# Optimization experiments

Measured on AMD Instinct MI355X. Metric: run time of the kernel, lower is better.

## Reference

```python
import jax, jax.numpy as jnp
import numpy as np

B, S, D, H = 64, 32, 1024, 1024


def setup_inputs() -> dict:
    key = jax.random.key(0)
    ks = jax.random.split(key, 12)
    sd = 1.0 / np.sqrt(D)
    sh = 1.0 / np.sqrt(H)
    return {
        "local_descs_t": jax.random.normal(ks[0], (B, S, D), jnp.float32),
        "local_descs_rot": jax.random.normal(ks[1], (B, S, D), jnp.float32),
        "scene_w": jax.random.normal(ks[2], (2 * D,), jnp.float32) * sd,
        "scene_b": jax.random.normal(ks[3], (1,), jnp.float32),
        "Wt1": jax.random.normal(ks[4], (S, D, H), jnp.float32) * sd,
        "bt1": jax.random.normal(ks[5], (S, H), jnp.float32) * 0.01,
        "Wt2": jax.random.normal(ks[6], (S, H, 3), jnp.float32) * sh,
        "bt2": jax.random.normal(ks[7], (S, 3), jnp.float32) * 0.01,
        "Wr1": jax.random.normal(ks[8], (S, D, H), jnp.float32) * sd,
        "br1": jax.random.normal(ks[9], (S, H), jnp.float32) * 0.01,
        "Wr2": jax.random.normal(ks[10], (S, H, 4), jnp.float32) * sh,
        "br2": jax.random.normal(ks[11], (S, 4), jnp.float32) * 0.01,
    }


def _pose_head(g, idx, W1, b1, W2, b2):
    # g: [B, D]; gather per-sample expert weights and run 2-layer MLP (GELU, exact erf as in F.gelu)
    h = jax.nn.gelu(jnp.einsum("bd,bdh->bh", g, W1[idx]) + b1[idx], approximate=False)
    return jnp.einsum("bh,bho->bo", h, W2[idx]) + b2[idx]


def reference(local_descs_t, local_descs_rot, scene_w, scene_b,
              Wt1, bt1, Wt2, bt2, Wr1, br1, Wr2, br2):
    # scene classification: Linear(2D -> 1) over concat descriptors, log-softmax over scenes
    logits = jnp.einsum("bsd,d->bs",
                        jnp.concatenate([local_descs_t, local_descs_rot], axis=2),
                        scene_w) + scene_b  # [B, S]
    scene_log_distr = jax.nn.log_softmax(logits, axis=1)
    idx = jnp.argmax(scene_log_distr, axis=1)  # top-1 scene per sample, [B]
    # select the chosen scene's descriptor (equivalent to one-hot mask * descs, summed over scenes)
    global_desc_t = jnp.take_along_axis(local_descs_t, idx[:, None, None], axis=1)[:, 0]    # [B, D]
    global_desc_rot = jnp.take_along_axis(local_descs_rot, idx[:, None, None], axis=1)[:, 0]
    # per-sample expert head dispatch (use_prior=False)
    x_t = _pose_head(global_desc_t, idx, Wt1, bt1, Wt2, bt2)      # [B, 3]
    x_rot = _pose_head(global_desc_rot, idx, Wr1, br1, Wr2, br2)  # [B, 4]
    expected_pose = jnp.concatenate([x_t, x_rot], axis=1)          # [B, 7]
    return expected_pose, scene_log_distr
```

## Files before the change

### kernel.cpp

```cpp
#include <hip/hip_runtime.h>
#include <math.h>

#define BB 64
#define SS 32
#define DD 1024
#define HH 1024
#define NG 40
#define GG 8

__device__ __forceinline__ float gelu_exact(float x) {
    return 0.5f * x * (1.0f + erff(x * 0.7071067811865476f));
}

#define WS_LOGITS 256
#define WS_GSCENE 8448
#define WS_GSAMP  8704
#define WS_PART   32768

__global__ __launch_bounds__(256) void logits_kernel(
    const float* __restrict__ descs_t, const float* __restrict__ descs_rot,
    const float* __restrict__ scene_w, float* __restrict__ logits)
{
    const int s = blockIdx.x, b = blockIdx.y;
    const int tid = threadIdx.x, lane = tid & 63, wave = tid >> 6;

    const float4* t4 = (const float4*)(descs_t  + ((size_t)b * SS + s) * DD);
    const float4* r4 = (const float4*)(descs_rot + ((size_t)b * SS + s) * DD);
    const float4* w4t = (const float4*)(scene_w);
    const float4* w4r = (const float4*)(scene_w + DD);

    float4 a = t4[tid], w = w4t[tid];
    float acc = a.x*w.x + a.y*w.y + a.z*w.z + a.w*w.w;
    float4 a2 = r4[tid], w2 = w4r[tid];
    acc += a2.x*w2.x + a2.y*w2.y + a2.z*w2.z + a2.w*w2.w;

    #pragma unroll
    for (int off = 32; off >= 1; off >>= 1) acc += __shfl_xor(acc, off, 64);

    __shared__ float red[4];
    if (lane == 0) red[wave] = acc;
    __syncthreads();
    if (tid == 0) logits[b * SS + s] = red[0] + red[1] + red[2] + red[3];
}

__global__ __launch_bounds__(64) void finalize_scene_kernel(
    const float* __restrict__ scene_b, float* __restrict__ logits,
    int* __restrict__ idx_ws, int* __restrict__ grp_scene, int* __restrict__ grp_samp,
    float* __restrict__ out)
{
    const int b = threadIdx.x;
    const float bias = scene_b[0];
    float lg[SS];
    float m = -1e30f; int am = 0;
    #pragma unroll
    for (int s = 0; s < SS; ++s) {
        lg[s] = logits[b * SS + s] + bias;
        if (lg[s] > m) { m = lg[s]; am = s; }
    }
    float sum = 0.f;
    #pragma unroll
    for (int s = 0; s < SS; ++s) sum += expf(lg[s] - m);
    const float lse = m + logf(sum);
    #pragma unroll
    for (int s = 0; s < SS; ++s) out[BB * 7 + b * SS + s] = lg[s] - lse;
    idx_ws[b] = am;

    __shared__ int sh_cnt[SS];
    __shared__ int sh_base[SS];
    __shared__ int sh_scene[NG];
    __shared__ int sh_samp[NG][GG];

    for (int i = b; i < NG; i += 64) sh_scene[i] = -1;
    for (int i = b; i < NG * GG; i += 64) ((int*)sh_samp)[i] = -1;

    int rank = 0;
    for (int s = 0; s < SS; ++s) {
        unsigned long long mk = __ballot(am == s);
        if (am == s) rank = __popcll(mk & ((1ull << b) - 1ull));
        if (b == s) sh_cnt[s] = (int)__popcll(mk);
    }
    __syncthreads();
    if (b == 0) {
        int acc = 0;
        for (int s = 0; s < SS; ++s) {
            sh_base[s] = acc;
            acc += (sh_cnt[s] + GG - 1) / GG;
        }
    }
    __syncthreads();
    {
        const int g = sh_base[am] + rank / GG;
        const int slot = rank % GG;
        sh_samp[g][slot] = b;
        if (slot == 0) sh_scene[g] = am;
    }
    __syncthreads();
    for (int i = b; i < NG; i += 64) grp_scene[i] = sh_scene[i];
    for (int i = b; i < NG * GG; i += 64) grp_samp[i] = ((int*)sh_samp)[i];
}

template<int DSPL>
__global__ __launch_bounds__(256) void layer1_kernel(
    const float* __restrict__ descs_t, const float* __restrict__ descs_rot,
    const float* __restrict__ Wt1, const float* __restrict__ Wr1,
    const int* __restrict__ grp_scene, const int* __restrict__ grp_samp,
    float* __restrict__ part)
{
    constexpr int DS = DD / DSPL;
    const int dsp  = blockIdx.x;
    const int g    = blockIdx.y;
    const int head = blockIdx.z;
    const int tid  = threadIdx.x;

    const int s = grp_scene[g];
    if (s < 0) return;

    __shared__ int   sh_b[GG];
    __shared__ float sh_g[DS][GG];
    if (tid < GG) sh_b[tid] = grp_samp[g * GG + tid];
    __syncthreads();

    const float* descs = head ? descs_rot : descs_t;
    for (int t = tid; t < GG * (DS / 4); t += 256) {
        const int p = t / (DS / 4);
        const int c = t % (DS / 4);
        const int b = sh_b[p];
        float4 v = make_float4(0.f, 0.f, 0.f, 0.f);
        if (b >= 0)
            v = ((const float4*)(descs + ((size_t)b * SS + s) * DD + dsp * DS))[c];
        sh_g[c * 4 + 0][p] = v.x;
        sh_g[c * 4 + 1][p] = v.y;
        sh_g[c * 4 + 2][p] = v.z;
        sh_g[c * 4 + 3][p] = v.w;
    }
    __syncthreads();

    const float* W = (head ? Wr1 : Wt1)
                   + (size_t)s * DD * HH + (size_t)dsp * DS * HH + tid * 4;

    float4 acc[GG];
    #pragma unroll
    for (int p = 0; p < GG; ++p) acc[p] = make_float4(0.f, 0.f, 0.f, 0.f);

    for (int d0 = 0; d0 < DS; d0 += 8) {
        float4 w[8];
        #pragma unroll
        for (int r = 0; r < 8; ++r)
            w[r] = *(const float4*)(W + (size_t)(d0 + r) * HH);
        #pragma unroll
        for (int r = 0; r < 8; ++r) {
            const float4 ga = *(const float4*)&sh_g[d0 + r][0];
            const float4 gb = *(const float4*)&sh_g[d0 + r][4];
            acc[0].x += ga.x*w[r].x; acc[0].y += ga.x*w[r].y; acc[0].z += ga.x*w[r].z; acc[0].w += ga.x*w[r].w;
            acc[1].x += ga.y*w[r].x; acc[1].y += ga.y*w[r].y; acc[1].z += ga.y*w[r].z; acc[1].w += ga.y*w[r].w;
            acc[2].x += ga.z*w[r].x; acc[2].y += ga.z*w[r].y; acc[2].z += ga.z*w[r].z; acc[2].w += ga.z*w[r].w;
            acc[3].x += ga.w*w[r].x; acc[3].y += ga.w*w[r].y; acc[3].z += ga.w*w[r].z; acc[3].w += ga.w*w[r].w;
            acc[4].x += gb.x*w[r].x; acc[4].y += gb.x*w[r].y; acc[4].z += gb.x*w[r].z; acc[4].w += gb.x*w[r].w;
            acc[5].x += gb.y*w[r].x; acc[5].y += gb.y*w[r].y; acc[5].z += gb.y*w[r].z; acc[5].w += gb.y*w[r].w;
            acc[6].x += gb.z*w[r].x; acc[6].y += gb.z*w[r].y; acc[6].z += gb.z*w[r].z; acc[6].w += gb.z*w[r].w;
            acc[7].x += gb.w*w[r].x; acc[7].y += gb.w*w[r].y; acc[7].z += gb.w*w[r].z; acc[7].w += gb.w*w[r].w;
        }
    }

    #pragma unroll
    for (int p = 0; p < GG; ++p) {
        const int b = sh_b[p];
        if (b >= 0) {
            float* dst = part + (((size_t)(head * BB + b) * DSPL + dsp) * HH) + tid * 4;
            *(float4*)dst = acc[p];
        }
    }
}

template<int DSPL>
__global__ __launch_bounds__(256) void head_out_kernel(
    const float* __restrict__ bt1, const float* __restrict__ Wt2, const float* __restrict__ bt2,
    const float* __restrict__ br1, const float* __restrict__ Wr2, const float* __restrict__ br2,
    const int* __restrict__ idx_ws, const float* __restrict__ part,
    float* __restrict__ out)
{
    const int b   = blockIdx.x;
    const int tid = threadIdx.x;
    const int s   = idx_ws[b];

    __shared__ float sh_h[2][HH];
    __shared__ float sh_red[7][4];

    #pragma unroll
    for (int head = 0; head < 2; ++head) {
        const float* b1 = (head ? br1 : bt1) + (size_t)s * HH;
        const float* p0 = part + ((size_t)(head * BB + b) * DSPL) * HH;
        const int j = tid * 4;
        float4 a = *(const float4*)(p0 + j);
        #pragma unroll
        for (int dsp = 1; dsp < DSPL; ++dsp) {
            float4 q = *(const float4*)(p0 + (size_t)dsp * HH + j);
            a.x += q.x; a.y += q.y; a.z += q.z; a.w += q.w;
        }
        float4 bb = *(const float4*)(b1 + j);
        sh_h[head][j + 0] = gelu_exact(a.x + bb.x);
        sh_h[head][j + 1] = gelu_exact(a.y + bb.y);
        sh_h[head][j + 2] = gelu_exact(a.z + bb.z);
        sh_h[head][j + 3] = gelu_exact(a.w + bb.w);
    }
    __syncthreads();

    const float* wt2 = Wt2 + (size_t)s * HH * 3;
    const float* wr2 = Wr2 + (size_t)s * HH * 4;
    float pa[7] = {0.f, 0.f, 0.f, 0.f, 0.f, 0.f, 0.f};
    for (int j = tid; j < HH; j += 256) {
        float ht = sh_h[0][j];
        float hr = sh_h[1][j];
        pa[0] += ht * wt2[j * 3 + 0];
        pa[1] += ht * wt2[j * 3 + 1];
        pa[2] += ht * wt2[j * 3 + 2];
        pa[3] += hr * wr2[j * 4 + 0];
        pa[4] += hr * wr2[j * 4 + 1];
        pa[5] += hr * wr2[j * 4 + 2];
        pa[6] += hr * wr2[j * 4 + 3];
    }
    const int lane = tid & 63, wave = tid >> 6;
    #pragma unroll
    for (int o = 0; o < 7; ++o) {
        float v = pa[o];
        #pragma unroll
        for (int off = 32; off >= 1; off >>= 1) v += __shfl_xor(v, off, 64);
        if (lane == 0) sh_red[o][wave] = v;
    }
    __syncthreads();
    if (tid < 7) {
        float v = sh_red[tid][0] + sh_red[tid][1] + sh_red[tid][2] + sh_red[tid][3];
        float bias = (tid < 3) ? bt2[(size_t)s * 3 + tid] : br2[(size_t)s * 4 + (tid - 3)];
        out[b * 7 + tid] = v + bias;
    }
}

template<int DSPL>
static void launch_pipeline(const float* descs_t, const float* descs_rot,
                            const float* Wt1, const float* Wr1,
                            const float* bt1, const float* Wt2, const float* bt2,
                            const float* br1, const float* Wr2, const float* br2,
                            int* idx_ws, int* grp_scene, int* grp_samp, float* part,
                            float* out, hipStream_t stream) {
    layer1_kernel<DSPL><<<dim3(DSPL, NG, 2), dim3(256), 0, stream>>>(
        descs_t, descs_rot, Wt1, Wr1, grp_scene, grp_samp, part);
    head_out_kernel<DSPL><<<dim3(BB), dim3(256), 0, stream>>>(
        bt1, Wt2, bt2, br1, Wr2, br2, idx_ws, part, out);
}

extern "C" void kernel_launch(void* const* d_in, const int* in_sizes, int n_in,
                              void* d_out, int out_size, void* d_ws, size_t ws_size,
                              hipStream_t stream) {
    const float* descs_t   = (const float*)d_in[0];
    const float* descs_rot = (const float*)d_in[1];
    const float* scene_w   = (const float*)d_in[2];
    const float* scene_b   = (const float*)d_in[3];
    const float* Wt1 = (const float*)d_in[4];
    const float* bt1 = (const float*)d_in[5];
    const float* Wt2 = (const float*)d_in[6];
    const float* bt2 = (const float*)d_in[7];
    const float* Wr1 = (const float*)d_in[8];
    const float* br1 = (const float*)d_in[9];
    const float* Wr2 = (const float*)d_in[10];
    const float* br2 = (const float*)d_in[11];
    float* out = (float*)d_out;

    int*   idx_ws    = (int*)d_ws;
    float* logits    = (float*)((char*)d_ws + WS_LOGITS);
    int*   grp_scene = (int*)((char*)d_ws + WS_GSCENE);
    int*   grp_samp  = (int*)((char*)d_ws + WS_GSAMP);
    float* part      = (float*)((char*)d_ws + WS_PART);

    logits_kernel<<<dim3(SS, BB), dim3(256), 0, stream>>>(
        descs_t, descs_rot, scene_w, logits);
    finalize_scene_kernel<<<dim3(1), dim3(64), 0, stream>>>(
        scene_b, logits, idx_ws, grp_scene, grp_samp, out);

    const size_t need16 = (size_t)WS_PART + (size_t)2 * BB * 16 * HH * sizeof(float);
    const size_t need8  = (size_t)WS_PART + (size_t)2 * BB * 8  * HH * sizeof(float);
    if (ws_size >= need16) {
        launch_pipeline<16>(descs_t, descs_rot, Wt1, Wr1, bt1, Wt2, bt2, br1, Wr2, br2,
                            idx_ws, grp_scene, grp_samp, part, out, stream);
    } else if (ws_size >= need8) {
        launch_pipeline<8>(descs_t, descs_rot, Wt1, Wr1, bt1, Wt2, bt2, br1, Wr2, br2,
                            idx_ws, grp_scene, grp_samp, part, out, stream);
    } else {
        launch_pipeline<4>(descs_t, descs_rot, Wt1, Wr1, bt1, Wt2, bt2, br1, Wr2, br2,
                            idx_ws, grp_scene, grp_samp, part, out, stream);
    }
}
```

Measured before the change: 56.65 us.

## Double-buffer weight loads in layer1 and add a 32-way D-split path

The layer1 GEMV loop now keeps two register buffers of weight rows. The next 8 rows are loaded while the current 8 are computed, and sched_barrier stops the compiler from reordering loads and FMAs, so global loads overlap with the arithmetic. A DSPL=32 pipeline is added when the workspace is large enough, raising the number of blocks in flight but doubling partial-sum traffic and reduction work in head_out. Register pressure rises from the second buffer. With DSPL=32 each block handles only 32 rows, so the loop is short.

```diff
diff --git a/kernel.cpp b/kernel.cpp
--- a/kernel.cpp
+++ b/kernel.cpp
@@ -98,6 +98,26 @@
     for (int i = b; i < NG; i += 64) grp_scene[i] = sh_scene[i];
     for (int i = b; i < NG * GG; i += 64) grp_samp[i] = ((int*)sh_samp)[i];
 }
+
+#define L1_LOAD(buf, base_row)                                             \
+    _Pragma("unroll")                                                      \
+    for (int r = 0; r < 8; ++r)                                            \
+        buf[r] = *(const float4*)(W + (size_t)((base_row) + r) * HH);
+
+#define L1_COMP(buf, base_row)                                             \
+    _Pragma("unroll")                                                      \
+    for (int r = 0; r < 8; ++r) {                                          \
+        const float4 ga = *(const float4*)&sh_g[(base_row) + r][0];        \
+        const float4 gb = *(const float4*)&sh_g[(base_row) + r][4];        \
+        acc[0].x += ga.x*buf[r].x; acc[0].y += ga.x*buf[r].y; acc[0].z += ga.x*buf[r].z; acc[0].w += ga.x*buf[r].w; \
+        acc[1].x += ga.y*buf[r].x; acc[1].y += ga.y*buf[r].y; acc[1].z += ga.y*buf[r].z; acc[1].w += ga.y*buf[r].w; \
+        acc[2].x += ga.z*buf[r].x; acc[2].y += ga.z*buf[r].y; acc[2].z += ga.z*buf[r].z; acc[2].w += ga.z*buf[r].w; \
+        acc[3].x += ga.w*buf[r].x; acc[3].y += ga.w*buf[r].y; acc[3].z += ga.w*buf[r].z; acc[3].w += ga.w*buf[r].w; \
+        acc[4].x += gb.x*buf[r].x; acc[4].y += gb.x*buf[r].y; acc[4].z += gb.x*buf[r].z; acc[4].w += gb.x*buf[r].w; \
+        acc[5].x += gb.y*buf[r].x; acc[5].y += gb.y*buf[r].y; acc[5].z += gb.y*buf[r].z; acc[5].w += gb.y*buf[r].w; \
+        acc[6].x += gb.z*buf[r].x; acc[6].y += gb.z*buf[r].y; acc[6].z += gb.z*buf[r].z; acc[6].w += gb.z*buf[r].w; \
+        acc[7].x += gb.w*buf[r].x; acc[7].y += gb.w*buf[r].y; acc[7].z += gb.w*buf[r].z; acc[7].w += gb.w*buf[r].w; \
+    }
 
 template<int DSPL>
 __global__ __launch_bounds__(256) void layer1_kernel(
@@ -142,25 +162,21 @@
     #pragma unroll
     for (int p = 0; p < GG; ++p) acc[p] = make_float4(0.f, 0.f, 0.f, 0.f);
 
-    for (int d0 = 0; d0 < DS; d0 += 8) {
-        float4 w[8];
-        #pragma unroll
-        for (int r = 0; r < 8; ++r)
-            w[r] = *(const float4*)(W + (size_t)(d0 + r) * HH);
-        #pragma unroll
-        for (int r = 0; r < 8; ++r) {
-            const float4 ga = *(const float4*)&sh_g[d0 + r][0];
-            const float4 gb = *(const float4*)&sh_g[d0 + r][4];
-            acc[0].x += ga.x*w[r].x; acc[0].y += ga.x*w[r].y; acc[0].z += ga.x*w[r].z; acc[0].w += ga.x*w[r].w;
-            acc[1].x += ga.y*w[r].x; acc[1].y += ga.y*w[r].y; acc[1].z += ga.y*w[r].z; acc[1].w += ga.y*w[r].w;
-            acc[2].x += ga.z*w[r].x; acc[2].y += ga.z*w[r].y; acc[2].z += ga.z*w[r].z; acc[2].w += ga.z*w[r].w;
-            acc[3].x += ga.w*w[r].x; acc[3].y += ga.w*w[r].y; acc[3].z += ga.w*w[r].z; acc[3].w += ga.w*w[r].w;
-            acc[4].x += gb.x*w[r].x; acc[4].y += gb.x*w[r].y; acc[4].z += gb.x*w[r].z; acc[4].w += gb.x*w[r].w;
-            acc[5].x += gb.y*w[r].x; acc[5].y += gb.y*w[r].y; acc[5].z += gb.y*w[r].z; acc[5].w += gb.y*w[r].w;
-            acc[6].x += gb.z*w[r].x; acc[6].y += gb.z*w[r].y; acc[6].z += gb.z*w[r].z; acc[6].w += gb.z*w[r].w;
-            acc[7].x += gb.w*w[r].x; acc[7].y += gb.w*w[r].y; acc[7].z += gb.w*w[r].z; acc[7].w += gb.w*w[r].w;
-        }
-    }
+    float4 wa[8], wb[8];
+    L1_LOAD(wa, 0);
+    L1_LOAD(wb, 8);
+    __builtin_amdgcn_sched_barrier(0);
+    #pragma unroll
+    for (int d0 = 0; d0 < DS - 16; d0 += 16) {
+        L1_COMP(wa, d0);
+        L1_LOAD(wa, d0 + 16);
+        __builtin_amdgcn_sched_barrier(0);
+        L1_COMP(wb, d0 + 8);
+        L1_LOAD(wb, d0 + 24);
+        __builtin_amdgcn_sched_barrier(0);
+    }
+    L1_COMP(wa, DS - 16);
+    L1_COMP(wb, DS - 8);
 
     #pragma unroll
     for (int p = 0; p < GG; ++p) {
@@ -192,7 +208,7 @@
         const float* p0 = part + ((size_t)(head * BB + b) * DSPL) * HH;
         const int j = tid * 4;
         float4 a = *(const float4*)(p0 + j);
-        #pragma unroll
+        #pragma unroll 8
         for (int dsp = 1; dsp < DSPL; ++dsp) {
             float4 q = *(const float4*)(p0 + (size_t)dsp * HH + j);
             a.x += q.x; a.y += q.y; a.z += q.z; a.w += q.w;
@@ -276,9 +292,13 @@
     finalize_scene_kernel<<<dim3(1), dim3(64), 0, stream>>>(
         scene_b, logits, idx_ws, grp_scene, grp_samp, out);
 
+    const size_t need32 = (size_t)WS_PART + (size_t)2 * BB * 32 * HH * sizeof(float);
     const size_t need16 = (size_t)WS_PART + (size_t)2 * BB * 16 * HH * sizeof(float);
     const size_t need8  = (size_t)WS_PART + (size_t)2 * BB * 8  * HH * sizeof(float);
-    if (ws_size >= need16) {
+    if (ws_size >= need32) {
+        launch_pipeline<32>(descs_t, descs_rot, Wt1, Wr1, bt1, Wt2, bt2, br1, Wr2, br2,
+                            idx_ws, grp_scene, grp_samp, part, out, stream);
+    } else if (ws_size >= need16) {
         launch_pipeline<16>(descs_t, descs_rot, Wt1, Wr1, bt1, Wt2, bt2, br1, Wr2, br2,
                             idx_ws, grp_scene, grp_samp, part, out, stream);
     } else if (ws_size >= need8) {
```

Measured after the change: 65.64 us. +15.9%, slower.
